# Kernel tuning notes

Measured on AMD Instinct MI355X. Metric: run time of the kernel, lower is better.

## Reference

```python
import jax, jax.numpy as jnp
import numpy as np
from jax import lax

SCALE = 2
K_UP = 5
BN_EPS = 1e-5
DN = ('NCHW', 'OIHW', 'NCHW')


def bn_eval(x, gamma, beta):
    # BatchNorm2d in eval mode with running_mean=0, running_var=1
    s = gamma / jnp.sqrt(1.0 + BN_EPS)
    return x * s[None, :, None, None] + beta[None, :, None, None]


def pixel_shuffle(x, r):
    b, C, h, w = x.shape
    c = C // (r * r)
    x = x.reshape(b, c, r, r, h, w)
    x = x.transpose(0, 1, 4, 2, 5, 3)  # b, c, h, r, w, r
    return x.reshape(b, c, h * r, w * r)


def setup_inputs() -> dict:
    key = jax.random.key(0)
    ks = jax.random.split(key, 3)
    b, c, h, w = 4, 128, 64, 64
    c_mid = 64
    return {
        'X': jax.random.normal(ks[0], (b, c, h, w), dtype=jnp.float32),
        'comp_w': jax.random.normal(ks[1], (c_mid, c, 1, 1), dtype=jnp.float32) * 0.05,
        'comp_g': jnp.ones((c_mid,), jnp.float32),
        'comp_b': jnp.zeros((c_mid,), jnp.float32),
        'enc_w': jax.random.normal(ks[2], ((SCALE * K_UP) ** 2, c_mid, 3, 3), dtype=jnp.float32) * 0.05,
        'enc_g': jnp.ones(((SCALE * K_UP) ** 2,), jnp.float32),
        'enc_b': jnp.zeros(((SCALE * K_UP) ** 2,), jnp.float32),
    }


def reference(X, comp_w, comp_g, comp_b, enc_w, enc_g, enc_b):
    b, c, h, w = X.shape
    h_, w_ = h * SCALE, w * SCALE
    pad = K_UP // 2 * SCALE  # = 4

    # comp: 1x1 conv + BN + SiLU
    W = lax.conv_general_dilated(X, comp_w, (1, 1), [(0, 0), (0, 0)], dimension_numbers=DN)
    W = jax.nn.silu(bn_eval(W, comp_g, comp_b))
    # enc: 3x3 conv (pad 1) + BN, no activation
    W = lax.conv_general_dilated(W, enc_w, (1, 1), [(1, 1), (1, 1)], dimension_numbers=DN)
    W = bn_eval(W, enc_g, enc_b)
    # pixel shuffle -> [b, k_up^2, h_, w_], softmax over kernel dim
    W = pixel_shuffle(W, SCALE)
    W = jax.nn.softmax(W, axis=1)

    # nearest-neighbor upsample of X
    Xu = jnp.repeat(jnp.repeat(X, SCALE, axis=2), SCALE, axis=3)  # [b, c, h_, w_]
    # unfold: kernel k_up, dilation=scale, padding=pad (im2col, channel-major)
    P = lax.conv_general_dilated_patches(
        Xu, (K_UP, K_UP), (1, 1), [(pad, pad), (pad, pad)],
        rhs_dilation=(SCALE, SCALE), dimension_numbers=DN)  # [b, c*k^2, h_, w_]
    P = P.reshape(b, c, K_UP * K_UP, h_, w_)

    return jnp.einsum('bkhw,bckhw->bchw', W, P)
```

## Files before the change

kernel.cpp:

```cpp
#include <hip/hip_runtime.h>
#include <hip/hip_bf16.h>
#include <math.h>

#define Bn   4
#define CIN  128
#define Hh   64
#define Ww   64
#define HW   4096
#define CMID 64
#define KOC  100
#define H2   128
#define W2d  128
#define HW2  16384
#define KUP  5
#define BN_EPS 1e-5f

typedef __attribute__((ext_vector_type(8)))  short  short8v;
typedef __attribute__((ext_vector_type(16))) float  float16v;

__device__ __forceinline__ ushort f2bf(float v) {
    __hip_bfloat16 h = __float2bfloat16(v);
    return *(ushort*)&h;
}

__global__ __launch_bounds__(256) void comp_kernel(
    const float* __restrict__ X,
    const float* __restrict__ cw,
    const float* __restrict__ cg,
    const float* __restrict__ cb,
    const float* __restrict__ ew,
    unsigned* __restrict__ W1b,
    ushort* __restrict__ Abf)
{
    int tid = threadIdx.x;
    if (blockIdx.x < 288) {
        int i   = blockIdx.x * 256 + tid;
        int cm  = i & 63;
        int kop = (i >> 6) & 127;
        int tap = i >> 13;
        float v = (kop < KOC) ? ew[((size_t)(kop * CMID + cm)) * 9 + tap] : 0.f;
        Abf[i] = f2bf(v);
    }

    int gt  = blockIdx.x * 256 + tid;
    int pg  = gt & 1023;
    int cog = (gt >> 10) & 31;
    int b   = gt >> 15;
    int pix = pg * 4;
    int co0 = cog * 2;

    const float* xb = X + (size_t)b * CIN * HW + pix;
    float4 acc0 = make_float4(0.f, 0.f, 0.f, 0.f);
    float4 acc1 = make_float4(0.f, 0.f, 0.f, 0.f);

#pragma unroll 4
    for (int ci = 0; ci < CIN; ++ci) {
        float4 xv = *(const float4*)(xb + (size_t)ci * HW);
        float w0 = cw[(size_t)co0 * CIN + ci];
        float w1 = cw[(size_t)(co0 + 1) * CIN + ci];
        acc0.x += xv.x * w0; acc0.y += xv.y * w0; acc0.z += xv.z * w0; acc0.w += xv.w * w0;
        acc1.x += xv.x * w1; acc1.y += xv.y * w1; acc1.z += xv.z * w1; acc1.w += xv.w * w1;
    }

    float inv_s = rsqrtf(1.0f + BN_EPS);
    float s0 = cg[co0] * inv_s,     bb0 = cb[co0];
    float s1 = cg[co0 + 1] * inv_s, bb1 = cb[co0 + 1];
    float r0[4] = {acc0.x, acc0.y, acc0.z, acc0.w};
    float r1[4] = {acc1.x, acc1.y, acc1.z, acc1.w};
#pragma unroll
    for (int i = 0; i < 4; ++i) {
        float v0 = r0[i] * s0 + bb0; v0 = v0 / (1.f + expf(-v0));
        float v1 = r1[i] * s1 + bb1; v1 = v1 / (1.f + expf(-v1));
        unsigned pk = (unsigned)f2bf(v0) | ((unsigned)f2bf(v1) << 16);
        W1b[((size_t)b * HW + pix + i) * 32 + cog] = pk;
    }
}

__global__ __launch_bounds__(256) void enc_kernel(
    const ushort* __restrict__ W1b_us,
    const ushort* __restrict__ Abf,
    const float* __restrict__ eg,
    const float* __restrict__ eb,
    float* __restrict__ Wsm)
{
    __shared__ float lsm[128 * 32];
    ushort* Bs = (ushort*)lsm;

    int bid   = blockIdx.x;
    int whalf = bid & 1;
    int h     = (bid >> 1) & 63;
    int b     = bid >> 7;
    int w0    = whalf * 32;
    int tid   = threadIdx.x;

    const unsigned* src  = (const unsigned*)W1b_us;
    unsigned*       dstu = (unsigned*)Bs;
    for (int i = tid; i < 3 * 34 * 32; i += 256) {
        int cp = i & 31;
        int t  = i >> 5;
        int wl = t % 34;
        int r  = t / 34;
        int gr = h - 1 + r, gw = w0 - 1 + wl;
        unsigned val = 0u;
        if ((unsigned)gr < 64u && (unsigned)gw < 64u)
            val = src[((size_t)b * HW + gr * 64 + gw) * 32 + cp];
        dstu[(r * 34 + wl) * 36 + cp] = val;
    }
    __syncthreads();

    int lane = tid & 63;
    int wid  = tid >> 6;
    int n    = lane & 31;
    int q    = lane >> 5;

    float16v acc;
#pragma unroll
    for (int i = 0; i < 16; ++i) acc[i] = 0.f;

    const ushort* Arow = Abf + ((size_t)(wid * 32 + n)) * 64 + q * 8;

#pragma unroll
    for (int tap = 0; tap < 9; ++tap) {
        int dy = tap / 3, dx = tap % 3;
        int bbase = ((dy * 34) + n + dx) * 72 + q * 8;
        const ushort* Atap = Arow + (size_t)tap * 128 * 64;
#pragma unroll
        for (int c = 0; c < 4; ++c) {
            short8v a = *(const short8v*)(Atap + c * 16);
            short8v bf = *(const short8v*)(Bs + bbase + c * 16);
            acc = __builtin_amdgcn_mfma_f32_32x32x16_bf16(a, bf, acc, 0, 0, 0);
        }
    }

    __syncthreads();

#pragma unroll
    for (int reg = 0; reg < 16; ++reg) {
        int row = (reg & 3) + 8 * (reg >> 2) + 4 * q;
        lsm[(wid * 32 + row) * 32 + n] = acc[reg];
    }
    __syncthreads();

    if (tid < 128) {
        int px  = tid & 31;
        int sub = tid >> 5;
        float inv_s = rsqrtf(1.0f + BN_EPS);
        float v[25];
        float m = -1e30f;
#pragma unroll
        for (int k = 0; k < 25; ++k) {
            int ko = 4 * k + sub;
            v[k] = lsm[ko * 32 + px] * (eg[ko] * inv_s) + eb[ko];
            m = fmaxf(m, v[k]);
        }
        float sum = 0.f;
#pragma unroll
        for (int k = 0; k < 25; ++k) {
            v[k] = expf(v[k] - m);
            sum += v[k];
        }
        float inv = 1.f / sum;
        float* po = Wsm + (size_t)b * KOC * HW + h * 64 + w0 + px;
#pragma unroll
        for (int k = 0; k < 25; ++k)
            po[(size_t)(4 * k + sub) * HW] = v[k] * inv;
    }
}

__global__ __launch_bounds__(256) void carafe_kernel(
    const float* __restrict__ X,
    const float* __restrict__ Wsm,
    float* __restrict__ out)
{
    __shared__ float wsm[4][25][32];

    int bid   = blockIdx.x;
    int whalf = bid & 1;
    int h     = (bid >> 1) & 63;
    int b     = bid >> 7;
    int w0    = whalf * 32;
    int tid   = threadIdx.x;

    const float* wsrc = Wsm + (size_t)b * KOC * HW + h * 64 + w0;
    for (int i = tid; i < 3200; i += 256) {
        int px = i & 31;
        int ko = i >> 5;
        wsm[ko & 3][ko >> 2][px] = wsrc[(size_t)ko * HW + px];
    }
    __syncthreads();

    int px  = tid & 31;
    int grp = tid >> 5;
    int w   = w0 + px;
    int c0  = grp * 16;

    float wt[100];
#pragma unroll
    for (int sub = 0; sub < 4; ++sub)
#pragma unroll
        for (int k = 0; k < 25; ++k)
            wt[sub * 25 + k] = wsm[sub][k][px];

    int off[25];
#pragma unroll
    for (int ki = 0; ki < 5; ++ki) {
#pragma unroll
        for (int kj = 0; kj < 5; ++kj) {
            int k = ki * 5 + kj;
            int r = h + ki - 2, cc = w + kj - 2;
            bool valid = ((unsigned)r < 64u) && ((unsigned)cc < 64u);
            int rc = r < 0 ? 0 : (r > 63 ? 63 : r);
            int cx = cc < 0 ? 0 : (cc > 63 ? 63 : cc);
            off[k] = rc * Ww + cx;
            if (!valid) { wt[k] = 0.f; wt[25+k] = 0.f; wt[50+k] = 0.f; wt[75+k] = 0.f; }
        }
    }

    const float* xp = X + ((size_t)b * CIN + c0) * HW;
    float* o0 = out + ((size_t)b * CIN + c0) * HW2 + (2 * h) * W2d + 2 * w;

    for (int c = 0; c < 16; ++c) {
        float x[25];
#pragma unroll
        for (int k = 0; k < 25; ++k) x[k] = xp[off[k]];
        float a0 = 0.f, a1 = 0.f, a2 = 0.f, a3 = 0.f;
#pragma unroll
        for (int k = 0; k < 25; ++k) {
            float xv = x[k];
            a0 += wt[k]      * xv;
            a1 += wt[25 + k] * xv;
            a2 += wt[50 + k] * xv;
            a3 += wt[75 + k] * xv;
        }
        *(float2*)o0          = make_float2(a0, a1);
        *(float2*)(o0 + W2d)  = make_float2(a2, a3);
        xp += HW;
        o0 += HW2;
    }
}

extern "C" void kernel_launch(void* const* d_in, const int* in_sizes, int n_in,
                              void* d_out, int out_size, void* d_ws, size_t ws_size,
                              hipStream_t stream)
{
    const float* X  = (const float*)d_in[0];
    const float* cw = (const float*)d_in[1];
    const float* cg = (const float*)d_in[2];
    const float* cb = (const float*)d_in[3];
    const float* ew = (const float*)d_in[4];
    const float* eg = (const float*)d_in[5];
    const float* eb = (const float*)d_in[6];
    float* out = (float*)d_out;

    char* ws = (char*)d_ws;
    unsigned* W1b = (unsigned*)ws;
    ushort*   Abf = (ushort*)(ws + 2097152);
    float*    Wsm = (float*)(ws + 2097152 + 147456);

    comp_kernel  <<<512, 256, 0, stream>>>(X, cw, cg, cb, ew, W1b, Abf);
    enc_kernel   <<<512, 256, 0, stream>>>((const ushort*)W1b, Abf, eg, eb, Wsm);
    carafe_kernel<<<512, 256, 0, stream>>>(X, Wsm, out);
}
```

Before: 137.6 us.

## Restructure carafe kernel to loop taps outer and split channels across blocks

The carafe kernel no longer keeps 100 weights and 25 offsets in registers per thread. It loops over the 25 taps, reads each tap's four sub-pixel weights as one float4 from a re-laid-out shared array, and accumulates 8 channels at once. Channel work is split across twice as many blocks, so each block handles 64 channels and each thread 8. This should cut register pressure and raise occupancy and load parallelism, at the cost of loading the weight tile twice per pixel row and keeping 32 accumulators live.

```diff
diff --git a/kernel.cpp b/kernel.cpp
--- a/kernel.cpp
+++ b/kernel.cpp
@@ -126,12 +126,11 @@
         const ushort* Atap = Arow + (size_t)tap * 128 * 64;
 #pragma unroll
         for (int c = 0; c < 4; ++c) {
-            short8v a = *(const short8v*)(Atap + c * 16);
+            short8v a  = *(const short8v*)(Atap + c * 16);
             short8v bf = *(const short8v*)(Bs + bbase + c * 16);
             acc = __builtin_amdgcn_mfma_f32_32x32x16_bf16(a, bf, acc, 0, 0, 0);
         }
     }
-
     __syncthreads();
 
 #pragma unroll
@@ -172,69 +171,65 @@
     const float* __restrict__ Wsm,
     float* __restrict__ out)
 {
-    __shared__ float wsm[4][25][32];
+    __shared__ float wsm2[25 * 32 * 4];
 
     int bid   = blockIdx.x;
-    int whalf = bid & 1;
-    int h     = (bid >> 1) & 63;
-    int b     = bid >> 7;
+    int chh   = bid & 1;
+    int whalf = (bid >> 1) & 1;
+    int h     = (bid >> 2) & 63;
+    int b     = bid >> 8;
     int w0    = whalf * 32;
     int tid   = threadIdx.x;
 
     const float* wsrc = Wsm + (size_t)b * KOC * HW + h * 64 + w0;
     for (int i = tid; i < 3200; i += 256) {
-        int px = i & 31;
-        int ko = i >> 5;
-        wsm[ko & 3][ko >> 2][px] = wsrc[(size_t)ko * HW + px];
+        int px_ = i & 31;
+        int ko  = i >> 5;
+        wsm2[((ko >> 2) * 32 + px_) * 4 + (ko & 3)] = wsrc[(size_t)ko * HW + px_];
     }
     __syncthreads();
 
     int px  = tid & 31;
     int grp = tid >> 5;
     int w   = w0 + px;
-    int c0  = grp * 16;
-
-    float wt[100];
-#pragma unroll
-    for (int sub = 0; sub < 4; ++sub)
-#pragma unroll
-        for (int k = 0; k < 25; ++k)
-            wt[sub * 25 + k] = wsm[sub][k][px];
-
-    int off[25];
-#pragma unroll
-    for (int ki = 0; ki < 5; ++ki) {
-#pragma unroll
-        for (int kj = 0; kj < 5; ++kj) {
-            int k = ki * 5 + kj;
-            int r = h + ki - 2, cc = w + kj - 2;
-            bool valid = ((unsigned)r < 64u) && ((unsigned)cc < 64u);
-            int rc = r < 0 ? 0 : (r > 63 ? 63 : r);
-            int cx = cc < 0 ? 0 : (cc > 63 ? 63 : cc);
-            off[k] = rc * Ww + cx;
-            if (!valid) { wt[k] = 0.f; wt[25+k] = 0.f; wt[50+k] = 0.f; wt[75+k] = 0.f; }
-        }
-    }
-
-    const float* xp = X + ((size_t)b * CIN + c0) * HW;
+    int c0  = chh * 64 + grp * 8;
+
+    float a0[8], a1[8], a2[8], a3[8];
+#pragma unroll
+    for (int c = 0; c < 8; ++c) { a0[c] = 0.f; a1[c] = 0.f; a2[c] = 0.f; a3[c] = 0.f; }
+
+    const float* xb = X + ((size_t)b * CIN + c0) * HW;
+
+#pragma unroll
+    for (int k = 0; k < 25; ++k) {
+        int ki = k / 5, kj = k % 5;
+        int r = h + ki - 2, cc = w + kj - 2;
+        float msk = (((unsigned)r < 64u) && ((unsigned)cc < 64u)) ? 1.f : 0.f;
+        int rc = r < 0 ? 0 : (r > 63 ? 63 : r);
+        int cx = cc < 0 ? 0 : (cc > 63 ? 63 : cc);
+        int off = rc * Ww + cx;
+
+        float4 wt4 = *(const float4*)&wsm2[(k * 32 + px) * 4];
+        float w0v = wt4.x * msk, w1v = wt4.y * msk;
+        float w2v = wt4.z * msk, w3v = wt4.w * msk;
+
+        float xv[8];
+#pragma unroll
+        for (int c = 0; c < 8; ++c) xv[c] = xb[(size_t)c * HW + off];
+#pragma unroll
+        for (int c = 0; c < 8; ++c) {
+            a0[c] += w0v * xv[c];
+            a1[c] += w1v * xv[c];
+            a2[c] += w2v * xv[c];
+            a3[c] += w3v * xv[c];
+        }
+    }
+
     float* o0 = out + ((size_t)b * CIN + c0) * HW2 + (2 * h) * W2d + 2 * w;
-
-    for (int c = 0; c < 16; ++c) {
-        float x[25];
-#pragma unroll
-        for (int k = 0; k < 25; ++k) x[k] = xp[off[k]];
-        float a0 = 0.f, a1 = 0.f, a2 = 0.f, a3 = 0.f;
-#pragma unroll
-        for (int k = 0; k < 25; ++k) {
-            float xv = x[k];
-            a0 += wt[k]      * xv;
-            a1 += wt[25 + k] * xv;
-            a2 += wt[50 + k] * xv;
-            a3 += wt[75 + k] * xv;
-        }
-        *(float2*)o0          = make_float2(a0, a1);
-        *(float2*)(o0 + W2d)  = make_float2(a2, a3);
-        xp += HW;
+#pragma unroll
+    for (int c = 0; c < 8; ++c) {
+        *(float2*)o0         = make_float2(a0[c], a1[c]);
+        *(float2*)(o0 + W2d) = make_float2(a2[c], a3[c]);
         o0 += HW2;
     }
 }
@@ -259,5 +254,5 @@
 
     comp_kernel  <<<512, 256, 0, stream>>>(X, cw, cg, cb, ew, W1b, Abf);
     enc_kernel   <<<512, 256, 0, stream>>>((const ushort*)W1b, Abf, eg, eb, Wsm);
-    carafe_kernel<<<512, 256, 0, stream>>>(X, Wsm, out);
-}
+    carafe_kernel<<<1024, 256, 0, stream>>>(X, Wsm, out);
+}
```

New measurement: 129.3 us. -6.0%, faster.
